# Performance work log

Hardware: AMD Instinct MI355X
Metric: run time of the kernel (lower is better)

The kernel has to match this reference:

```python
import jax, jax.numpy as jnp
import numpy as np

B, S, D, I, C = 4, 512, 512, 1024, 64
BASE_LR = 0.01
EPS = 1e-6


def _rms(x, w):
    return x * jax.lax.rsqrt(jnp.mean(x * x, axis=-1, keepdims=True) + EPS) * w


def _mem_apply(p, x):
    # 2-layer MLP memory: x + RMSNorm(W1 @ silu(W0 @ x))
    h = jax.nn.silu(x @ p["w0"].T)
    y = h @ p["w1"].T
    return x + _rms(y, p["ln"])


def _mem_loss(p, inp, tgt, w):
    # ((target - pred)^2 * theta).mean(-1).sum() over batch; w is scalar theta_t
    pred = _mem_apply(p, inp)
    return jnp.sum(jnp.mean((tgt - pred) ** 2 * w, axis=-1))


def _neural_memory(x, wq, wk, wv, q_norm_w, k_norm_w, alpha_w, alpha_b,
                   theta_w, theta_b, eta_w, eta_b, m_w0, m_w1, m_ln):
    b, s, d = x.shape
    nC = s // C
    params0 = {"w0": m_w0, "w1": m_w1, "ln": m_ln}
    surpr0 = jax.tree_util.tree_map(jnp.zeros_like, params0)
    xs = x.reshape(b, nC, C, d).transpose(1, 0, 2, 3)  # [nC, B, C, D]

    # per-token grads: vmap over sequence dim 1, shared params (in_dims=None)
    grad_fn = jax.vmap(jax.grad(_mem_loss), in_axes=(None, 1, 1, 0))
    idx = jnp.arange(C)

    def step(carry, xc):
        params, surpr = carry
        # adaptive gates: Linear -> sum over batch -> sigmoid (shapes [C])
        al = jax.nn.sigmoid(jnp.sum(xc @ alpha_w.T + alpha_b, axis=0))[:, 0]
        th = jax.nn.sigmoid(jnp.sum(xc @ theta_w.T + theta_b, axis=0))[:, 0] * BASE_LR
        et = jax.nn.sigmoid(jnp.sum(xc @ eta_w.T + eta_b, axis=0))[:, 0]
        k = _rms(jax.nn.silu(xc @ wk.T), k_norm_w)  # [B, C, D]
        v = jax.nn.silu(xc @ wv.T)
        grads = grad_fn(params, k, v, th)  # each leaf [C, *param_shape]
        # eta decay matrix E[m,n] = prod_{i=n+1}^m eta_i for n<=m, else 0
        M0 = jnp.where(idx[:, None] > idx[None, :], et[:, None], 1.0)
        Emat = jnp.where(idx[None, :] <= idx[:, None], jnp.cumprod(M0, axis=0), 0.0)
        c_eta = jnp.cumprod(et)  # prod_{0..m} eta
        beta = 1.0 - al
        bc_last = jnp.cumprod(beta)[-1]
        bt = jnp.cumprod(beta[::-1])[::-1]  # bt[m] = prod_{m..C-1} beta
        w_beta = jnp.concatenate([bt[1:], jnp.ones((1,), et.dtype)])

        def upd(pS, pM, u):
            # S_t = eta_t * S_{t-1} - u_t ; M_t = beta_t * M_{t-1} + S_t (vectorized)
            ex = (slice(None),) + (None,) * pS.ndim
            S_all = c_eta[ex] * pS - jnp.einsum("mn,n...->m...", Emat, u)
            newM = pM * bc_last + jnp.einsum("m,m...->...", w_beta, S_all)
            return newM, S_all[-1]

        res = {n: upd(surpr[n], params[n], grads[n]) for n in params}
        new_params = {n: res[n][0] for n in params}
        new_surpr = {n: res[n][1] for n in params}
        return (new_params, new_surpr), None

    (paramsF, _surprF), _ = jax.lax.scan(step, (params0, surpr0), xs)
    # retrieve from updated memory
    q = _rms(jax.nn.silu(x @ wq.T), q_norm_w)
    return _mem_apply(paramsF, q)


def setup_inputs() -> dict:
    key = jax.random.key(0)
    ks = jax.random.split(key, 12)

    def xavier(k, shape):
        lim = float(np.sqrt(6.0 / (shape[0] + shape[1])))
        return jax.random.uniform(k, shape, jnp.float32, -lim, lim)

    return {
        "x": jax.random.normal(ks[0], (B, S, D), jnp.float32),
        "wq": xavier(ks[1], (D, D)),
        "wk": xavier(ks[2], (D, D)),
        "wv": xavier(ks[3], (D, D)),
        "q_norm_w": jnp.ones((D,), jnp.float32),
        "k_norm_w": jnp.ones((D,), jnp.float32),
        "alpha_w": xavier(ks[4], (1, D)),
        "alpha_b": jnp.zeros((1,), jnp.float32),
        "theta_w": xavier(ks[5], (1, D)),
        "theta_b": jnp.zeros((1,), jnp.float32),
        "eta_w": xavier(ks[6], (1, D)),
        "eta_b": jnp.zeros((1,), jnp.float32),
        "m_w0": xavier(ks[7], (I, D)),
        "m_w1": xavier(ks[8], (D, I)),
        "m_ln": jnp.ones((D,), jnp.float32),
    }


def reference(x, wq, wk, wv, q_norm_w, k_norm_w, alpha_w, alpha_b,
              theta_w, theta_b, eta_w, eta_b, m_w0, m_w1, m_ln):
    return _neural_memory(x, wq, wk, wv, q_norm_w, k_norm_w, alpha_w, alpha_b,
                          theta_w, theta_b, eta_w, eta_b, m_w0, m_w1, m_ln)
```

## Files before the change

kernel.cpp:

```cpp
#include <hip/hip_runtime.h>
#include <math.h>

#define EPS 1e-6f

namespace {

typedef unsigned short u16;
typedef unsigned int u32;
typedef __bf16 bf16x8 __attribute__((ext_vector_type(8)));
typedef float f32x4 __attribute__((ext_vector_type(4)));
typedef u16 u16x8 __attribute__((ext_vector_type(8)));

constexpr int Bb = 4, Ss = 512, Dd = 512, Ii = 1024, Cc = 64;
constexpr int nCk = 8, RowsC = 256, RowsAll = 2048;

__device__ __forceinline__ float sigmoidf_(float x) { return 1.f / (1.f + expf(-x)); }
__device__ __forceinline__ float siluf_(float x)    { return x / (1.f + expf(-x)); }

__device__ __forceinline__ u16 f2bf(float f) {
  u32 u = __float_as_uint(f);
  u32 r = u + 0x7fffu + ((u >> 16) & 1u);
  return (u16)(r >> 16);
}
__device__ __forceinline__ float bf2f(u16 u) {
  return __uint_as_float(((u32)u) << 16);
}

__device__ __forceinline__ void llds16(const u16* g, u16* l) {
  __builtin_amdgcn_global_load_lds((__attribute__((address_space(1))) void*)g,
                                   (__attribute__((address_space(3))) void*)l,
                                   16, 0, 0);
}

__device__ __forceinline__ void drain_barrier() {
  asm volatile("s_waitcnt vmcnt(0)" ::: "memory");
  __builtin_amdgcn_s_barrier();
}

__device__ __forceinline__ float wave_sum(float v) {
  #pragma unroll
  for (int m = 32; m > 0; m >>= 1) v += __shfl_xor(v, m, 64);
  return v;
}

__device__ __forceinline__ float block_reduce_sum(float v, float* red) {
  int tid = threadIdx.x;
  red[tid] = v; __syncthreads();
  for (int s = 128; s > 0; s >>= 1) {
    if (tid < s) red[tid] += red[tid + s];
    __syncthreads();
  }
  float r = red[0]; __syncthreads();
  return r;
}

struct WS {
  float *w0c, *Sw0, *w1c, *Sw1, *lnc, *Sln, *tmpK, *Krows, *Vrows,
        *Ybuf, *gyr, *alv, *thv, *etv, *wBv, *wEv, *scal, *Qb, *Yr;
  u16 *xcb, *wkvqb, *w0b, *w1b, *w1tb, *Kb, *KT, *Hb, *Ht, *dZb,
      *dYb, *dYtW, *dYtE, *dHtW, *dHtE, *Qbb, *Hrb;
};
__host__ __device__ inline WS mkws(char* base) {
  WS s; char* p = base + 256;
#define CF(nm, n) s.nm = (float*)p; p += (size_t)(n) * 4;
#define CU(nm, n) s.nm = (u16*)p;   p += (size_t)(n) * 2;
  CF(w0c, Ii*Dd) CF(Sw0, Ii*Dd) CF(w1c, Dd*Ii) CF(Sw1, Dd*Ii)
  CF(lnc, Dd) CF(Sln, Dd)
  CF(tmpK, (size_t)RowsAll*Dd) CF(Krows, (size_t)RowsAll*Dd) CF(Vrows, (size_t)RowsAll*Dd)
  CF(Ybuf, RowsC*Dd) CF(gyr, RowsC*Dd)
  CF(alv, Ss) CF(thv, Ss) CF(etv, Ss) CF(wBv, nCk*RowsC) CF(wEv, nCk*RowsC) CF(scal, nCk*4)
  CF(Qb, (size_t)RowsAll*Dd) CF(Yr, (size_t)RowsAll*Dd)
  CU(xcb, (size_t)RowsAll*Dd) CU(wkvqb, (size_t)3*Dd*Dd)
  CU(w0b, (size_t)Ii*Dd) CU(w1b, (size_t)2*Dd*Ii) CU(w1tb, (size_t)2*Ii*Dd)
  CU(Kb, (size_t)RowsAll*Dd) CU(KT, (size_t)RowsAll*Dd)
  CU(Hb, RowsC*Ii) CU(Ht, RowsC*Ii) CU(dZb, RowsC*Ii)
  CU(dYb, RowsC*Dd) CU(dYtW, RowsC*Dd) CU(dYtE, RowsC*Dd)
  CU(dHtW, RowsC*Ii) CU(dHtE, RowsC*Ii)
  CU(Qbb, (size_t)RowsAll*Dd) CU(Hrb, (size_t)RowsAll*Ii)
#undef CF
#undef CU
  return s;
}

template<int BK, int NBUF, int EPI>
__device__ void tile64(
    u16* smA, u16* smB,
    const u16* __restrict__ A, const u16* __restrict__ Bt,
    int K, int N, int bm, int bn,
    float* C0, float* C1, float* C2,
    u16* Cb, u16* CbT, u16* CbT2,
    const u16* Zb, const float* wB, const float* wE, int trM)
{
  constexpr int CPR = BK / 8;
  constexpr int NISS = (64 * CPR) / 256;
  constexpr int BUF = 64 * BK;
  const int tid = threadIdx.x;
  const int l = tid & 63, lr = l & 15, lq = l >> 4;
  const int w = tid >> 6, wr = w >> 1, wc = w & 1;

  f32x4 acc[2][2];
  #pragma unroll
  for (int i = 0; i < 2; ++i)
    #pragma unroll
    for (int j = 0; j < 2; ++j) acc[i][j] = f32x4{0.f, 0.f, 0.f, 0.f};

  auto stage = [&](int k0, int buf) {
    u16* dA = smA + buf * BUF;
    u16* dB = smB + buf * BUF;
    #pragma unroll
    for (int i = 0; i < NISS; ++i) {
      int e = i * 256 + tid;
      int r = e / CPR, c = (e & (CPR - 1)) ^ (r & (CPR - 1));
      llds16(A  + (size_t)(bm + r) * K + k0 + c * 8, dA + e * 8);
      llds16(Bt + (size_t)(bn + r) * K + k0 + c * 8, dB + e * 8);
    }
  };

  stage(0, 0);
  drain_barrier();
  const int nt = K / BK;
  int cur = 0;
  for (int t = 0; t < nt; ++t) {
    if (t + 1 < nt) stage((t + 1) * BK, (cur ^ 1) & (NBUF - 1));
    const u16* sA = smA + cur * BUF;
    const u16* sB = smB + cur * BUF;
    #pragma unroll
    for (int kk = 0; kk < BK / 32; ++kk) {
      bf16x8 av[2], bv[2];
      #pragma unroll
      for (int m = 0; m < 2; ++m) {
        int r = wr * 32 + m * 16 + lr;
        int c = (kk * 4 + lq) ^ (r & (CPR - 1));
        av[m] = *reinterpret_cast<const bf16x8*>(&sA[r * BK + c * 8]);
      }
      #pragma unroll
      for (int n = 0; n < 2; ++n) {
        int r = wc * 32 + n * 16 + lr;
        int c = (kk * 4 + lq) ^ (r & (CPR - 1));
        bv[n] = *reinterpret_cast<const bf16x8*>(&sB[r * BK + c * 8]);
      }
      #pragma unroll
      for (int m = 0; m < 2; ++m)
        #pragma unroll
        for (int n = 0; n < 2; ++n)
          acc[m][n] = __builtin_amdgcn_mfma_f32_16x16x32_bf16(av[m], bv[n], acc[m][n], 0, 0, 0);
    }
    drain_barrier();
    cur = (cur ^ 1) & (NBUF - 1);
  }

  #pragma unroll
  for (int m = 0; m < 2; ++m) {
    int gr0 = bm + wr * 32 + m * 16 + lq * 4;
    float wbq[4], weq[4];
    if (EPI == 3) {
      #pragma unroll
      for (int q = 0; q < 4; ++q) { wbq[q] = wB[gr0 + q]; weq[q] = wE[gr0 + q]; }
    }
    #pragma unroll
    for (int n = 0; n < 2; ++n) {
      int gc = bn + wc * 32 + n * 16 + lr;
      ushort4 t1, t2;
      #pragma unroll
      for (int q = 0; q < 4; ++q) {
        float v = acc[m][n][q];
        size_t idx = (size_t)(gr0 + q) * N + gc;
        if (EPI == 0) {
          C0[idx] = v;
        } else if (EPI == 1) {
          size_t rb = (size_t)(gr0 + q) * Dd;
          if (gc < Dd)            C0[rb + gc] = v;
          else if (gc < 2 * Dd)   C1[rb + gc - Dd] = siluf_(v);
          else                    C2[rb + gc - 2 * Dd] = v;
        } else if (EPI == 2) {
          float sg = 1.f / (1.f + expf(-v));
          float h = v * sg;
          float ds = sg * (1.f + v * (1.f - sg));
          Cb[idx] = f2bf(h);
          CbT2[idx] = f2bf(ds);
          ((u16*)&t1)[q] = f2bf(h);
        } else if (EPI == 3) {
          float dh = v * bf2f(Zb[idx]);
          ((u16*)&t1)[q] = f2bf(dh * wbq[q]);
          ((u16*)&t2)[q] = f2bf(dh * weq[q]);
        } else if (EPI == 4) {
          Cb[idx] = f2bf(siluf_(v));
        }
      }
      if (EPI == 2) *reinterpret_cast<ushort4*>(&CbT[(size_t)gc * trM + gr0]) = t1;
      if (EPI == 3) {
        *reinterpret_cast<ushort4*>(&CbT[(size_t)gc * trM + gr0]) = t1;
        *reinterpret_cast<ushort4*>(&CbT2[(size_t)gc * trM + gr0]) = t2;
      }
    }
  }
}

template<int BK, int NBUF, bool TR>
__device__ void gtile64(
    u16* smA, u16* smB, u16* smE,
    const u16* __restrict__ AW, const u16* __restrict__ AE,
    const u16* __restrict__ Bt,
    float* P, float* Sm, u16* Pb, u16* PbT, const float* scal,
    int M, int N, int K, int bm, int bn)
{
  constexpr int CPR = BK / 8;
  constexpr int NISS = (64 * CPR) / 256;
  constexpr int BUF = 64 * BK;
  const int tid = threadIdx.x;
  const int l = tid & 63, lr = l & 15, lq = l >> 4;
  const int w = tid >> 6, wr = w >> 1, wc = w & 1;

  f32x4 aM[2][2], aE[2][2];
  #pragma unroll
  for (int i = 0; i < 2; ++i)
    #pragma unroll
    for (int j = 0; j < 2; ++j) {
      aM[i][j] = f32x4{0.f, 0.f, 0.f, 0.f};
      aE[i][j] = f32x4{0.f, 0.f, 0.f, 0.f};
    }

  auto stage = [&](int k0, int buf) {
    u16* dA = smA + buf * BUF;
    u16* dE = smE + buf * BUF;
    u16* dB = smB + buf * BUF;
    #pragma unroll
    for (int i = 0; i < NISS; ++i) {
      int e = i * 256 + tid;
      int r = e / CPR, c = (e & (CPR - 1)) ^ (r & (CPR - 1));
      llds16(AW + (size_t)(bm + r) * K + k0 + c * 8, dA + e * 8);
      llds16(AE + (size_t)(bm + r) * K + k0 + c * 8, dE + e * 8);
      llds16(Bt + (size_t)(bn + r) * K + k0 + c * 8, dB + e * 8);
    }
  };

  stage(0, 0);
  drain_barrier();
  const int nt = K / BK;
  int cur = 0;
  for (int t = 0; t < nt; ++t) {
    if (t + 1 < nt) stage((t + 1) * BK, (cur ^ 1) & (NBUF - 1));
    const u16* sA = smA + cur * BUF;
    const u16* sE = smE + cur * BUF;
    const u16* sB = smB + cur * BUF;
    #pragma unroll
    for (int kk = 0; kk < BK / 32; ++kk) {
      bf16x8 awv[2], aev[2], bv[2];
      #pragma unroll
      for (int m = 0; m < 2; ++m) {
        int r = wr * 32 + m * 16 + lr;
        int c = (kk * 4 + lq) ^ (r & (CPR - 1));
        awv[m] = *reinterpret_cast<const bf16x8*>(&sA[r * BK + c * 8]);
        aev[m] = *reinterpret_cast<const bf16x8*>(&sE[r * BK + c * 8]);
      }
      #pragma unroll
      for (int n = 0; n < 2; ++n) {
        int r = wc * 32 + n * 16 + lr;
        int c = (kk * 4 + lq) ^ (r & (CPR - 1));
        bv[n] = *reinterpret_cast<const bf16x8*>(&sB[r * BK + c * 8]);
      }
      #pragma unroll
      for (int m = 0; m < 2; ++m)
        #pragma unroll
        for (int n = 0; n < 2; ++n) {
          aM[m][n] = __builtin_amdgcn_mfma_f32_16x16x32_bf16(awv[m], bv[n], aM[m][n], 0, 0, 0);
          aE[m][n] = __builtin_amdgcn_mfma_f32_16x16x32_bf16(aev[m], bv[n], aE[m][n], 0, 0, 0);
        }
    }
    drain_barrier();
    cur = (cur ^ 1) & (NBUF - 1);
  }

  float s0 = scal[0], s1 = scal[1], s2 = scal[2];
  #pragma unroll
  for (int m = 0; m < 2; ++m) {
    int gr0 = bm + wr * 32 + m * 16 + lq * 4;
    #pragma unroll
    for (int n = 0; n < 2; ++n) {
      int gc = bn + wc * 32 + n * 16 + lr;
      ushort4 t1;
      #pragma unroll
      for (int q = 0; q < 4; ++q) {
        size_t idx = (size_t)(gr0 + q) * N + gc;
        float p = P[idx], s = Sm[idx];
        float np = s0 * p + s1 * s - aM[m][n][q];
        float ns = s2 * s - aE[m][n][q];
        P[idx] = np; Sm[idx] = ns;
        Pb[idx] = f2bf(np);
        if (TR) ((u16*)&t1)[q] = f2bf(np);
      }
      if (TR) *reinterpret_cast<ushort4*>(&PbT[(size_t)gc * M + gr0]) = t1;
    }
  }
}


__global__ __launch_bounds__(256) void z0_k(
    const u16* __restrict__ A, const u16* __restrict__ Bt,
    u16* Hb, u16* Ht, u16* dZb)
{
  __shared__ __align__(16) u16 sm[4 * 64 * 128];
  tile64<128, 2, 2>(sm, sm + 2 * 64 * 128, A, Bt, Dd, Ii,
                    blockIdx.y * 64, blockIdx.x * 64,
                    nullptr, nullptr, nullptr, Hb, Ht, dZb,
                    nullptr, nullptr, nullptr, RowsC);
}

__global__ __launch_bounds__(256) void y_k(
    const u16* __restrict__ A, const u16* __restrict__ Bt, float* C0)
{
  __shared__ __align__(16) u16 sm[4 * 64 * 128];
  tile64<128, 2, 0>(sm, sm + 2 * 64 * 128, A, Bt, Ii, Dd,
                    blockIdx.y * 64, blockIdx.x * 64,
                    C0, nullptr, nullptr, nullptr, nullptr, nullptr,
                    nullptr, nullptr, nullptr, 0);
}

__global__ __launch_bounds__(256) void s4_k(
    const u16* __restrict__ dYb, const u16* __restrict__ w1t_cur,
    const u16* __restrict__ dZb, u16* dHtW, u16* dHtE,
    const float* __restrict__ gyr, float* lnc, float* Sln,
    const u16* __restrict__ dYtW, const u16* __restrict__ dYtE,
    const u16* __restrict__ Ht,
    float* w1c, float* Sw1, u16* w1b_new, u16* w1t_new,
    const float* wB, const float* wE, const float* scal)
{
  __shared__ __align__(16) u16 sm[6 * 64 * 128];
  int j = blockIdx.x;
  if (j < 64) {
    int tm = j & 3, tn = j >> 2;
    tile64<128, 2, 3>(sm, sm + 2 * 64 * 128, dYb, w1t_cur, Dd, Ii,
                      tm * 64, tn * 64,
                      nullptr, nullptr, nullptr, nullptr, dHtW, dHtE,
                      dZb, wB, wE, RowsC);
  } else if (j < 66) {
    int d = (j - 64) * 256 + threadIdx.x;
    float sm2 = 0.f, se2 = 0.f;
    for (int r = 0; r < RowsC; ++r) {
      float vv = gyr[(size_t)r * Dd + d];
      sm2 += wB[r] * vv; se2 += wE[r] * vv;
    }
    float pp = lnc[d], sn = Sln[d];
    lnc[d] = scal[0] * pp + scal[1] * sn - sm2;
    Sln[d] = scal[2] * sn - se2;
  } else {
    int q = j - 66;
    gtile64<128, 2, true>(sm, sm + 2 * 64 * 128, sm + 4 * 64 * 128,
                          dYtW, dYtE, Ht, w1c, Sw1, w1b_new, w1t_new,
                          scal, Dd, Ii, RowsC, (q >> 4) * 64, (q & 15) * 64);
  }
}

__global__ __launch_bounds__(256) void g2b_k(
    const u16* __restrict__ dHtW, const u16* __restrict__ dHtE,
    const u16* __restrict__ KTc,
    float* w0c, float* Sw0, u16* w0b, const float* scal)
{
  __shared__ __align__(16) u16 sm[6 * 64 * 128];
  int j = blockIdx.x;
  gtile64<128, 2, false>(sm, sm + 2 * 64 * 128, sm + 4 * 64 * 128,
                         dHtW, dHtE, KTc, w0c, Sw0, w0b, nullptr,
                         scal, Ii, Dd, RowsC, (j >> 3) * 64, (j & 7) * 64);
}

__global__ __launch_bounds__(256) void kvq_k(
    const u16* __restrict__ xcb, const u16* __restrict__ wkvqb,
    float* tmpK, float* Vrows, float* Yq, char* ws)
{
  __shared__ __align__(16) u16 sm[4 * 64 * 128];
  int j = blockIdx.x;
  if (j < 768) {
    int tn = j % 24, tm = j / 24;
    tile64<128, 2, 1>(sm, sm + 2 * 64 * 128, xcb, wkvqb, Dd, 3 * Dd,
                      tm * 64, tn * 64,
                      tmpK, Vrows, Yq, nullptr, nullptr, nullptr,
                      nullptr, nullptr, nullptr, 0);
    return;
  }
  if (threadIdx.x != 0) return;
  WS S = mkws(ws);
  int ci = j - 768;
  const float* alc = S.alv + ci * Cc;
  const float* etc_ = S.etv + ci * Cc;
  float beta[Cc], wb[Cc], ce[Cc], E[Cc], T[Cc];
  for (int i = 0; i < Cc; ++i) beta[i] = 1.f - alc[i];
  wb[Cc - 1] = 1.f;
  for (int m = Cc - 2; m >= 0; --m) wb[m] = wb[m + 1] * beta[m + 1];
  float bc_last = wb[0] * beta[0];
  float p = 1.f, A = 0.f;
  for (int m = 0; m < Cc; ++m) { p *= etc_[m]; ce[m] = p; A += wb[m] * ce[m]; }
  E[Cc - 1] = 1.f; T[Cc - 1] = 1.f;
  for (int n = Cc - 2; n >= 0; --n) {
    E[n] = E[n + 1] * etc_[n + 1];
    T[n] = wb[n] + etc_[n + 1] * T[n + 1];
  }
  for (int b = 0; b < Bb; ++b)
    for (int t = 0; t < Cc; ++t) {
      S.wBv[ci * RowsC + b * Cc + t] = T[t];
      S.wEv[ci * RowsC + b * Cc + t] = E[t];
    }
  S.scal[ci * 4 + 0] = bc_last; S.scal[ci * 4 + 1] = A; S.scal[ci * 4 + 2] = ce[Cc - 1];
}

template<int EPI>
__global__ __launch_bounds__(256) void mgemm128_k(
    const u16* __restrict__ A, const u16* __restrict__ Bt,
    float* C0, u16* Cb, int M, int N, int K)
{
  constexpr int TS = 128, BK = 64;
  constexpr int BUF = TS * BK;
  __shared__ __align__(16) u16 As[2 * BUF];
  __shared__ __align__(16) u16 Bs[2 * BUF];
  const int tid = threadIdx.x;
  const int l = tid & 63, lr = l & 15, lq = l >> 4;
  const int w = tid >> 6, wr = w >> 1, wc = w & 1;
  const int bm = blockIdx.y * TS, bn = blockIdx.x * TS;

  f32x4 acc[4][4];
  #pragma unroll
  for (int i = 0; i < 4; ++i)
    #pragma unroll
    for (int j = 0; j < 4; ++j) acc[i][j] = f32x4{0.f, 0.f, 0.f, 0.f};

  auto stage = [&](int k0, int buf) {
    u16* dA = As + buf * BUF;
    u16* dB = Bs + buf * BUF;
    #pragma unroll
    for (int i = 0; i < 4; ++i) {
      int e = i * 256 + tid;
      int r = e >> 3, c = (e & 7) ^ (r & 7);
      llds16(A  + (size_t)(bm + r) * K + k0 + c * 8, dA + e * 8);
      llds16(Bt + (size_t)(bn + r) * K + k0 + c * 8, dB + e * 8);
    }
  };

  stage(0, 0);
  drain_barrier();
  const int nt = K / BK;
  int cur = 0;
  for (int t = 0; t < nt; ++t) {
    if (t + 1 < nt) stage((t + 1) * BK, cur ^ 1);
    const u16* sA = As + cur * BUF;
    const u16* sB = Bs + cur * BUF;
    #pragma unroll
    for (int kk = 0; kk < 2; ++kk) {
      bf16x8 av[4], bv[4];
      #pragma unroll
      for (int m = 0; m < 4; ++m) {
        int r = wr * 64 + m * 16 + lr;
        int c = (kk * 4 + lq) ^ (r & 7);
        av[m] = *reinterpret_cast<const bf16x8*>(&sA[r * BK + c * 8]);
      }
      #pragma unroll
      for (int n = 0; n < 4; ++n) {
        int r = wc * 64 + n * 16 + lr;
        int c = (kk * 4 + lq) ^ (r & 7);
        bv[n] = *reinterpret_cast<const bf16x8*>(&sB[r * BK + c * 8]);
      }
      #pragma unroll
      for (int m = 0; m < 4; ++m)
        #pragma unroll
        for (int n = 0; n < 4; ++n)
          acc[m][n] = __builtin_amdgcn_mfma_f32_16x16x32_bf16(av[m], bv[n], acc[m][n], 0, 0, 0);
    }
    drain_barrier();
    cur ^= 1;
  }

  #pragma unroll
  for (int m = 0; m < 4; ++m) {
    int gr0 = bm + wr * 64 + m * 16 + lq * 4;
    #pragma unroll
    for (int n = 0; n < 4; ++n) {
      int gc = bn + wc * 64 + n * 16 + lr;
      #pragma unroll
      for (int q = 0; q < 4; ++q) {
        size_t idx = (size_t)(gr0 + q) * N + gc;
        float v = acc[m][n][q];
        if (EPI == 0) C0[idx] = v;
        else          Cb[idx] = f2bf(siluf_(v));
      }
    }
  }
}

__global__ __launch_bounds__(256) void init_k(
    const float* __restrict__ x,
    const float* __restrict__ aw, const float* __restrict__ ab,
    const float* __restrict__ tw, const float* __restrict__ tb,
    const float* __restrict__ ew, const float* __restrict__ eb,
    const float* __restrict__ wq, const float* __restrict__ wkw,
    const float* __restrict__ wvw, const float* __restrict__ mw0,
    const float* __restrict__ mw1, const float* __restrict__ mln,
    char* ws)
{
  WS S = mkws(ws);
  const int tid = threadIdx.x;
  if (blockIdx.x < 512) {
    __shared__ float red[256];
    int s = blockIdx.x;
    int ci = s >> 6, t = s & 63;
    float sa = 0.f, st = 0.f, se = 0.f;
    for (int b = 0; b < Bb; ++b) {
      const float* xr = x + ((size_t)b * Ss + s) * Dd;
      u16* dst = S.xcb + ((size_t)(ci * RowsC + b * Cc + t)) * Dd;
      for (int d = tid; d < Dd; d += 256) {
        float v = xr[d];
        dst[d] = f2bf(v);
        sa += v * aw[d]; st += v * tw[d]; se += v * ew[d];
      }
    }
    sa = block_reduce_sum(sa, red);
    st = block_reduce_sum(st, red);
    se = block_reduce_sum(se, red);
    if (tid == 0) {
      S.alv[s] = sigmoidf_(sa + Bb * ab[0]);
      S.thv[s] = sigmoidf_(st + Bb * tb[0]) * 0.01f;
      S.etv[s] = sigmoidf_(se + Bb * eb[0]);
    }
    return;
  }
  if (blockIdx.x < 640) {
    __shared__ float t[64][65];
    int tt = blockIdx.x - 512;
    int br = (tt & 7) * 64, bc = (tt >> 3) * 64;
    #pragma unroll
    for (int i = 0; i < 16; ++i) {
      int e = tid + i * 256;
      int r = e >> 6, c = e & 63;
      t[r][c] = mw1[(size_t)(br + r) * Ii + bc + c];
    }
    __syncthreads();
    #pragma unroll
    for (int i = 0; i < 16; ++i) {
      int e = tid + i * 256;
      int rr = e >> 6, cc = e & 63;
      S.w1tb[(size_t)(bc + rr) * Dd + br + cc] = f2bf(t[cc][rr]);
    }
    return;
  }
  const int i0 = (blockIdx.x - 640) * 256 + tid;
  const int stride = 512 * 256;
  for (int i = i0; i < (Dd * Dd) / 4; i += stride) {
    float4 v = ((const float4*)wkw)[i];
    ushort4 o; o.x = f2bf(v.x); o.y = f2bf(v.y); o.z = f2bf(v.z); o.w = f2bf(v.w);
    ((ushort4*)S.wkvqb)[i] = o;
    v = ((const float4*)wvw)[i];
    o.x = f2bf(v.x); o.y = f2bf(v.y); o.z = f2bf(v.z); o.w = f2bf(v.w);
    ((ushort4*)S.wkvqb)[i + (Dd * Dd) / 4] = o;
    v = ((const float4*)wq)[i];
    o.x = f2bf(v.x); o.y = f2bf(v.y); o.z = f2bf(v.z); o.w = f2bf(v.w);
    ((ushort4*)S.wkvqb)[i + (Dd * Dd) / 2] = o;
  }
  for (int i = i0; i < (Ii * Dd) / 4; i += stride) {
    float4 z4; z4.x = z4.y = z4.z = z4.w = 0.f;
    float4 v = ((const float4*)mw0)[i];
    ((float4*)S.w0c)[i] = v; ((float4*)S.Sw0)[i] = z4;
    ushort4 o; o.x = f2bf(v.x); o.y = f2bf(v.y); o.z = f2bf(v.z); o.w = f2bf(v.w);
    ((ushort4*)S.w0b)[i] = o;
    v = ((const float4*)mw1)[i];
    ((float4*)S.w1c)[i] = v; ((float4*)S.Sw1)[i] = z4;
    o.x = f2bf(v.x); o.y = f2bf(v.y); o.z = f2bf(v.z); o.w = f2bf(v.w);
    ((ushort4*)S.w1b)[i] = o;
  }
  for (int i = i0; i < Dd; i += stride) { S.lnc[i] = mln[i]; S.Sln[i] = 0.f; }
}

__global__ __launch_bounds__(256) void norm2_k(
    const float* __restrict__ tmpK, const float* __restrict__ Yq,
    float* Krows, u16* Kb, u16* KT,
    float* Qb, u16* Qbb,
    const float* __restrict__ kn, const float* __restrict__ qn)
{
  __shared__ u16 lt[4][Dd];
  const int tid = threadIdx.x, w = tid >> 6, l = tid & 63;
  const bool isQ = blockIdx.x >= 512;
  const int r0 = (isQ ? (int)blockIdx.x - 512 : (int)blockIdx.x) * 4;
  const int row = r0 + w, d0 = l * 8;
  const float* in = (isQ ? Yq : tmpK) + (size_t)row * Dd + d0;
  const float* nw = (isQ ? qn : kn) + d0;
  float v[8];
  *(float4*)&v[0] = *(const float4*)in;
  *(float4*)&v[4] = *(const float4*)(in + 4);
  float ss = 0.f;
  #pragma unroll
  for (int j = 0; j < 8; ++j) { v[j] = siluf_(v[j]); ss += v[j] * v[j]; }
  ss = wave_sum(ss);
  float rr = rsqrtf(ss / (float)Dd + EPS);
  float nv[8];
  *(float4*)&nv[0] = *(const float4*)nw;
  *(float4*)&nv[4] = *(const float4*)(nw + 4);
  float y[8]; u16x8 pb;
  #pragma unroll
  for (int j = 0; j < 8; ++j) { y[j] = v[j] * rr * nv[j]; pb[j] = f2bf(y[j]); }
  float* outf = (isQ ? Qb : Krows) + (size_t)row * Dd + d0;
  u16* outb = (isQ ? Qbb : Kb) + (size_t)row * Dd + d0;
  *(float4*)outf       = *(float4*)&y[0];
  *(float4*)(outf + 4) = *(float4*)&y[4];
  *(u16x8*)outb = pb;
  if (!isQ) {
    int ci = r0 >> 8, rloc = r0 & 255;
    u16* KTc = KT + (size_t)ci * Dd * RowsC;
    #pragma unroll
    for (int j = 0; j < 8; ++j) lt[w][d0 + j] = pb[j];
    __syncthreads();
    for (int d = tid; d < Dd; d += 256) {
      ushort4 pk;
      pk.x = lt[0][d]; pk.y = lt[1][d]; pk.z = lt[2][d]; pk.w = lt[3][d];
      *reinterpret_cast<ushort4*>(&KTc[(size_t)d * RowsC + rloc]) = pk;
    }
  }
}

__global__ __launch_bounds__(256) void loss_back4_k(
    const float* __restrict__ Kr, const float* __restrict__ Vr,
    const float* __restrict__ Y, const float* __restrict__ lnc,
    const float* __restrict__ th, const float* __restrict__ wB,
    const float* __restrict__ wE,
    u16* __restrict__ dYb, u16* __restrict__ dYtW, u16* __restrict__ dYtE,
    float* __restrict__ gyr)
{
  __shared__ u16 lw[4][Dd];
  __shared__ u16 le[4][Dd];
  const int tid = threadIdx.x, w = tid >> 6, l = tid & 63;
  const int row = blockIdx.x * 4 + w, t = row & 63, d0 = l * 8;
  size_t base = (size_t)row * Dd + d0;

  float y[8], kk[8], vv[8], lv[8];
  *(float4*)&y[0]  = *(const float4*)(Y + base);
  *(float4*)&y[4]  = *(const float4*)(Y + base + 4);
  *(float4*)&kk[0] = *(const float4*)(Kr + base);
  *(float4*)&kk[4] = *(const float4*)(Kr + base + 4);
  *(float4*)&vv[0] = *(const float4*)(Vr + base);
  *(float4*)&vv[4] = *(const float4*)(Vr + base + 4);
  *(float4*)&lv[0] = *(const float4*)(lnc + d0);
  *(float4*)&lv[4] = *(const float4*)(lnc + d0 + 4);

  float ss = 0.f;
  #pragma unroll
  for (int q = 0; q < 8; ++q) ss += y[q] * y[q];
  ss = wave_sum(ss);
  float rr = rsqrtf(ss / (float)Dd + EPS);
  float c = 2.f * th[t] / (float)Dd;

  float g[8], s2 = 0.f;
  #pragma unroll
  for (int q = 0; q < 8; ++q) {
    g[q] = c * ((kk[q] + y[q] * rr * lv[q]) - vv[q]);
    s2 += g[q] * lv[q] * y[q];
  }
  s2 = wave_sum(s2);
  float coef = rr * rr * rr * s2 / (float)Dd;

  float wb = wB[row], we = wE[row];
  u16x8 pb; float gy[8];
  #pragma unroll
  for (int q = 0; q < 8; ++q) {
    float dv = rr * g[q] * lv[q] - coef * y[q];
    pb[q] = f2bf(dv);
    lw[w][d0 + q] = f2bf(dv * wb);
    le[w][d0 + q] = f2bf(dv * we);
    gy[q] = g[q] * y[q] * rr;
  }
  *(u16x8*)(dYb + base) = pb;
  *(float4*)(gyr + base)     = *(float4*)&gy[0];
  *(float4*)(gyr + base + 4) = *(float4*)&gy[4];

  __syncthreads();
  int r0 = blockIdx.x * 4;
  for (int d = tid; d < Dd; d += 256) {
    ushort4 pw, pe;
    pw.x = lw[0][d]; pw.y = lw[1][d]; pw.z = lw[2][d]; pw.w = lw[3][d];
    pe.x = le[0][d]; pe.y = le[1][d]; pe.z = le[2][d]; pe.w = le[3][d];
    *reinterpret_cast<ushort4*>(&dYtW[(size_t)d * RowsC + r0]) = pw;
    *reinterpret_cast<ushort4*>(&dYtE[(size_t)d * RowsC + r0]) = pe;
  }
}

__global__ __launch_bounds__(256) void final4_k(
    const float* __restrict__ Q, const float* __restrict__ Y,
    const float* __restrict__ lnc, float* __restrict__ out)
{
  const int tid = threadIdx.x, w = tid >> 6, l = tid & 63;
  const int row = blockIdx.x * 4 + w;
  const int ci = row >> 8, wi = row & 255, b = wi >> 6, t = wi & 63;
  const int d0 = l * 8;
  const float* yr = Y + (size_t)row * Dd + d0;
  float y[8];
  *(float4*)&y[0] = *(const float4*)yr;
  *(float4*)&y[4] = *(const float4*)(yr + 4);
  float ss = 0.f;
  #pragma unroll
  for (int q = 0; q < 8; ++q) ss += y[q] * y[q];
  ss = wave_sum(ss);
  float rr = rsqrtf(ss / (float)Dd + EPS);
  const float* qb = Q + (size_t)row * Dd + d0;
  const float* lf = lnc + d0;
  float o[8];
  #pragma unroll
  for (int q = 0; q < 8; ++q) o[q] = qb[q] + y[q] * rr * lf[q];
  float* ob = out + ((size_t)b * Ss + ci * Cc + t) * Dd + d0;
  *(float4*)ob       = *(float4*)&o[0];
  *(float4*)(ob + 4) = *(float4*)&o[4];
}

}

extern "C" void kernel_launch(void* const* d_in, const int* in_sizes, int n_in,
                              void* d_out, int out_size, void* d_ws, size_t ws_size,
                              hipStream_t stream)
{
  const float* x   = (const float*)d_in[0];
  const float* wq  = (const float*)d_in[1];
  const float* wkw = (const float*)d_in[2];
  const float* wvw = (const float*)d_in[3];
  const float* qn  = (const float*)d_in[4];
  const float* kn  = (const float*)d_in[5];
  const float* aw  = (const float*)d_in[6];
  const float* ab  = (const float*)d_in[7];
  const float* tw  = (const float*)d_in[8];
  const float* tb  = (const float*)d_in[9];
  const float* ew  = (const float*)d_in[10];
  const float* eb  = (const float*)d_in[11];
  const float* mw0 = (const float*)d_in[12];
  const float* mw1 = (const float*)d_in[13];
  const float* mln = (const float*)d_in[14];
  float* out = (float*)d_out;
  char* ws = (char*)d_ws;
  WS S = mkws(ws);

  init_k<<<1152, 256, 0, stream>>>(x, aw, ab, tw, tb, ew, eb,
                                   wq, wkw, wvw, mw0, mw1, mln, ws);
  kvq_k<<<776, 256, 0, stream>>>(S.xcb, S.wkvqb, S.tmpK, S.Vrows, S.Yr, ws);
  norm2_k<<<1024, 256, 0, stream>>>(S.tmpK, S.Yr, S.Krows, S.Kb, S.KT,
                                    S.Qb, S.Qbb, kn, qn);

  for (int ci = 0; ci < nCk; ++ci) {
    const int p = ci & 1;
    const u16* Kbc = S.Kb + (size_t)ci * RowsC * Dd;
    const u16* KTc = S.KT + (size_t)ci * Dd * RowsC;
    const float* Krc = S.Krows + (size_t)ci * RowsC * Dd;
    const float* Vrc = S.Vrows + (size_t)ci * RowsC * Dd;
    const float* scc = S.scal + ci * 4;
    const float* wBc = S.wBv + ci * RowsC;
    const float* wEc = S.wEv + ci * RowsC;
    const float* thc = S.thv + ci * Cc;
    u16* w1b_cur = S.w1b + (size_t)p * Dd * Ii;
    u16* w1b_new = S.w1b + (size_t)(p ^ 1) * Dd * Ii;
    u16* w1t_cur = S.w1tb + (size_t)p * Ii * Dd;
    u16* w1t_new = S.w1tb + (size_t)(p ^ 1) * Ii * Dd;

    z0_k<<<dim3(Ii / 64, RowsC / 64), 256, 0, stream>>>(
        Kbc, S.w0b, S.Hb, S.Ht, S.dZb);
    y_k<<<dim3(Dd / 64, RowsC / 64), 256, 0, stream>>>(
        S.Hb, w1b_cur, S.Ybuf);
    loss_back4_k<<<RowsC / 4, 256, 0, stream>>>(
        Krc, Vrc, S.Ybuf, S.lnc, thc, wBc, wEc, S.dYb, S.dYtW, S.dYtE, S.gyr);
    s4_k<<<194, 256, 0, stream>>>(
        S.dYb, w1t_cur, S.dZb, S.dHtW, S.dHtE, S.gyr, S.lnc, S.Sln,
        S.dYtW, S.dYtE, S.Ht, S.w1c, S.Sw1, w1b_new, w1t_new,
        wBc, wEc, scc);
    g2b_k<<<128, 256, 0, stream>>>(
        S.dHtW, S.dHtE, KTc, S.w0c, S.Sw0, S.w0b, scc);
  }

  mgemm128_k<4><<<dim3(Ii / 128, RowsAll / 128), 256, 0, stream>>>(
      S.Qbb, S.w0b, nullptr, S.Hrb, RowsAll, Ii, Dd);
  mgemm128_k<0><<<dim3(Dd / 128, RowsAll / 128), 256, 0, stream>>>(
      S.Hrb, S.w1b, S.Yr, nullptr, RowsAll, Dd, Ii);
  final4_k<<<RowsAll / 4, 256, 0, stream>>>(S.Qb, S.Yr, S.lnc, out);
}
```

Baseline: 394.9 us.

## Fuse hidden-layer GEMM and output GEMM per chunk with split-K partial sums

Merges the z0 (K·W0ᵀ with SiLU epilogue) and y (H·W1ᵀ) kernels into one kernel. Each block computes a 64x64 H tile, keeps it in shared memory, and multiplies it by the matching 64-column slice of W1 to produce a full-width partial Y. Sixteen partials are written to a scratch buffer and summed in loss_back4_k. This removes one launch and the H round trip through global memory. In exchange it writes and reads 16x more fp32 Y partial data, and the second GEMM runs on only 64 blocks with large register accumulators.

```diff
diff --git a/kernel.cpp b/kernel.cpp
--- a/kernel.cpp
+++ b/kernel.cpp
@@ -56,8 +56,8 @@
 
 struct WS {
   float *w0c, *Sw0, *w1c, *Sw1, *lnc, *Sln, *tmpK, *Krows, *Vrows,
-        *Ybuf, *gyr, *alv, *thv, *etv, *wBv, *wEv, *scal, *Qb, *Yr;
-  u16 *xcb, *wkvqb, *w0b, *w1b, *w1tb, *Kb, *KT, *Hb, *Ht, *dZb,
+        *Yp, *gyr, *alv, *thv, *etv, *wBv, *wEv, *scal, *Qb, *Yr;
+  u16 *xcb, *wkvqb, *w0b, *w1b, *w1tb, *Kb, *KT, *Ht, *dZb,
       *dYb, *dYtW, *dYtE, *dHtW, *dHtE, *Qbb, *Hrb;
 };
 __host__ __device__ inline WS mkws(char* base) {
@@ -67,13 +67,13 @@
   CF(w0c, Ii*Dd) CF(Sw0, Ii*Dd) CF(w1c, Dd*Ii) CF(Sw1, Dd*Ii)
   CF(lnc, Dd) CF(Sln, Dd)
   CF(tmpK, (size_t)RowsAll*Dd) CF(Krows, (size_t)RowsAll*Dd) CF(Vrows, (size_t)RowsAll*Dd)
-  CF(Ybuf, RowsC*Dd) CF(gyr, RowsC*Dd)
+  CF(Yp, (size_t)16*RowsC*Dd) CF(gyr, RowsC*Dd)
   CF(alv, Ss) CF(thv, Ss) CF(etv, Ss) CF(wBv, nCk*RowsC) CF(wEv, nCk*RowsC) CF(scal, nCk*4)
   CF(Qb, (size_t)RowsAll*Dd) CF(Yr, (size_t)RowsAll*Dd)
   CU(xcb, (size_t)RowsAll*Dd) CU(wkvqb, (size_t)3*Dd*Dd)
   CU(w0b, (size_t)Ii*Dd) CU(w1b, (size_t)2*Dd*Ii) CU(w1tb, (size_t)2*Ii*Dd)
   CU(Kb, (size_t)RowsAll*Dd) CU(KT, (size_t)RowsAll*Dd)
-  CU(Hb, RowsC*Ii) CU(Ht, RowsC*Ii) CU(dZb, RowsC*Ii)
+  CU(Ht, RowsC*Ii) CU(dZb, RowsC*Ii)
   CU(dYb, RowsC*Dd) CU(dYtW, RowsC*Dd) CU(dYtE, RowsC*Dd)
   CU(dHtW, RowsC*Ii) CU(dHtE, RowsC*Ii)
   CU(Qbb, (size_t)RowsAll*Dd) CU(Hrb, (size_t)RowsAll*Ii)
@@ -88,7 +88,7 @@
     const u16* __restrict__ A, const u16* __restrict__ Bt,
     int K, int N, int bm, int bn,
     float* C0, float* C1, float* C2,
-    u16* Cb, u16* CbT, u16* CbT2,
+    u16* CbT, u16* CbT2,
     const u16* Zb, const float* wB, const float* wE, int trM)
 {
   constexpr int CPR = BK / 8;
@@ -172,22 +172,12 @@
           if (gc < Dd)            C0[rb + gc] = v;
           else if (gc < 2 * Dd)   C1[rb + gc - Dd] = siluf_(v);
           else                    C2[rb + gc - 2 * Dd] = v;
-        } else if (EPI == 2) {
-          float sg = 1.f / (1.f + expf(-v));
-          float h = v * sg;
-          float ds = sg * (1.f + v * (1.f - sg));
-          Cb[idx] = f2bf(h);
-          CbT2[idx] = f2bf(ds);
-          ((u16*)&t1)[q] = f2bf(h);
         } else if (EPI == 3) {
           float dh = v * bf2f(Zb[idx]);
           ((u16*)&t1)[q] = f2bf(dh * wbq[q]);
           ((u16*)&t2)[q] = f2bf(dh * weq[q]);
-        } else if (EPI == 4) {
-          Cb[idx] = f2bf(siluf_(v));
         }
       }
-      if (EPI == 2) *reinterpret_cast<ushort4*>(&CbT[(size_t)gc * trM + gr0]) = t1;
       if (EPI == 3) {
         *reinterpret_cast<ushort4*>(&CbT[(size_t)gc * trM + gr0]) = t1;
         *reinterpret_cast<ushort4*>(&CbT2[(size_t)gc * trM + gr0]) = t2;
@@ -295,25 +285,147 @@
 }
 
 
-__global__ __launch_bounds__(256) void z0_k(
-    const u16* __restrict__ A, const u16* __restrict__ Bt,
-    u16* Hb, u16* Ht, u16* dZb)
-{
-  __shared__ __align__(16) u16 sm[4 * 64 * 128];
-  tile64<128, 2, 2>(sm, sm + 2 * 64 * 128, A, Bt, Dd, Ii,
-                    blockIdx.y * 64, blockIdx.x * 64,
-                    nullptr, nullptr, nullptr, Hb, Ht, dZb,
-                    nullptr, nullptr, nullptr, RowsC);
-}
-
-__global__ __launch_bounds__(256) void y_k(
-    const u16* __restrict__ A, const u16* __restrict__ Bt, float* C0)
-{
-  __shared__ __align__(16) u16 sm[4 * 64 * 128];
-  tile64<128, 2, 0>(sm, sm + 2 * 64 * 128, A, Bt, Ii, Dd,
-                    blockIdx.y * 64, blockIdx.x * 64,
-                    C0, nullptr, nullptr, nullptr, nullptr, nullptr,
-                    nullptr, nullptr, nullptr, 0);
+__global__ __launch_bounds__(256) void z0y_k(
+    const u16* __restrict__ Kbc, const u16* __restrict__ w0b,
+    const u16* __restrict__ w1b,
+    u16* __restrict__ Ht, u16* __restrict__ dZb, float* __restrict__ Yp)
+{
+  __shared__ __align__(16) u16 sm[4 * 64 * 128 + 64 * 64];
+  u16* Hs = sm + 4 * 64 * 128;
+  const int tid = threadIdx.x;
+  const int l = tid & 63, lr = l & 15, lq = l >> 4;
+  const int w = tid >> 6, wr = w >> 1, wc = w & 1;
+  const int tj = blockIdx.x, tr = blockIdx.y;
+  const int bm = tr * 64, bn = tj * 64;
+
+  {
+    constexpr int BK = 128, CPR = 16, NISS = 4, BUF = 64 * BK;
+    u16* smA = sm; u16* smB = sm + 2 * BUF;
+    f32x4 acc[2][2];
+    #pragma unroll
+    for (int i = 0; i < 2; ++i)
+      #pragma unroll
+      for (int j = 0; j < 2; ++j) acc[i][j] = f32x4{0.f, 0.f, 0.f, 0.f};
+
+    auto stage = [&](int k0, int buf) {
+      u16* dA = smA + buf * BUF;
+      u16* dB = smB + buf * BUF;
+      #pragma unroll
+      for (int i = 0; i < NISS; ++i) {
+        int e = i * 256 + tid;
+        int r = e / CPR, c = (e & (CPR - 1)) ^ (r & (CPR - 1));
+        llds16(Kbc + (size_t)(bm + r) * Dd + k0 + c * 8, dA + e * 8);
+        llds16(w0b + (size_t)(bn + r) * Dd + k0 + c * 8, dB + e * 8);
+      }
+    };
+    stage(0, 0);
+    drain_barrier();
+    int cur = 0;
+    for (int t = 0; t < 4; ++t) {
+      if (t + 1 < 4) stage((t + 1) * BK, cur ^ 1);
+      const u16* sA = smA + cur * BUF;
+      const u16* sB = smB + cur * BUF;
+      #pragma unroll
+      for (int kk = 0; kk < 4; ++kk) {
+        bf16x8 av[2], bv[2];
+        #pragma unroll
+        for (int m = 0; m < 2; ++m) {
+          int r = wr * 32 + m * 16 + lr;
+          int c = (kk * 4 + lq) ^ (r & (CPR - 1));
+          av[m] = *reinterpret_cast<const bf16x8*>(&sA[r * BK + c * 8]);
+        }
+        #pragma unroll
+        for (int n = 0; n < 2; ++n) {
+          int r = wc * 32 + n * 16 + lr;
+          int c = (kk * 4 + lq) ^ (r & (CPR - 1));
+          bv[n] = *reinterpret_cast<const bf16x8*>(&sB[r * BK + c * 8]);
+        }
+        #pragma unroll
+        for (int m = 0; m < 2; ++m)
+          #pragma unroll
+          for (int n = 0; n < 2; ++n)
+            acc[m][n] = __builtin_amdgcn_mfma_f32_16x16x32_bf16(av[m], bv[n], acc[m][n], 0, 0, 0);
+      }
+      drain_barrier();
+      cur ^= 1;
+    }
+
+    #pragma unroll
+    for (int i = 0; i < 16; ++i) {
+      int e = i * 256 + tid;
+      int r = e >> 3, c = (e & 7) ^ (r & 7);
+      llds16(w1b + (size_t)r * Ii + bn + c * 8, sm + e * 8);
+    }
+
+    #pragma unroll
+    for (int m = 0; m < 2; ++m) {
+      int gr0 = bm + wr * 32 + m * 16 + lq * 4;
+      int rl0 = wr * 32 + m * 16 + lq * 4;
+      #pragma unroll
+      for (int n = 0; n < 2; ++n) {
+        int gc = bn + wc * 32 + n * 16 + lr;
+        int cl = wc * 32 + n * 16 + lr;
+        ushort4 t1;
+        #pragma unroll
+        for (int q = 0; q < 4; ++q) {
+          float v = acc[m][n][q];
+          float sg = 1.f / (1.f + expf(-v));
+          float h = v * sg;
+          float ds = sg * (1.f + v * (1.f - sg));
+          u16 hb = f2bf(h);
+          ((u16*)&t1)[q] = hb;
+          dZb[(size_t)(gr0 + q) * Ii + gc] = f2bf(ds);
+          int rl = rl0 + q;
+          Hs[rl * 64 + ((((cl >> 3) ^ (rl & 7)) << 3) | (cl & 7))] = hb;
+        }
+        *reinterpret_cast<ushort4*>(&Ht[(size_t)gc * RowsC + gr0]) = t1;
+      }
+    }
+  }
+
+  asm volatile("s_waitcnt vmcnt(0)" ::: "memory");
+  __syncthreads();
+
+  {
+    f32x4 yacc[2][16];
+    #pragma unroll
+    for (int m = 0; m < 2; ++m)
+      #pragma unroll
+      for (int n = 0; n < 16; ++n) yacc[m][n] = f32x4{0.f, 0.f, 0.f, 0.f};
+
+    #pragma unroll
+    for (int kk = 0; kk < 2; ++kk) {
+      bf16x8 av[2];
+      #pragma unroll
+      for (int m = 0; m < 2; ++m) {
+        int r = wr * 32 + m * 16 + lr;
+        int c = (kk * 4 + lq) ^ (r & 7);
+        av[m] = *reinterpret_cast<const bf16x8*>(&Hs[r * 64 + c * 8]);
+      }
+      #pragma unroll
+      for (int n = 0; n < 16; ++n) {
+        int r = wc * 256 + n * 16 + lr;
+        int c = (kk * 4 + lq) ^ (r & 7);
+        bf16x8 bv = *reinterpret_cast<const bf16x8*>(&sm[r * 64 + c * 8]);
+        #pragma unroll
+        for (int m = 0; m < 2; ++m)
+          yacc[m][n] = __builtin_amdgcn_mfma_f32_16x16x32_bf16(av[m], bv, yacc[m][n], 0, 0, 0);
+      }
+    }
+
+    float* Yo = Yp + (size_t)tj * RowsC * Dd;
+    #pragma unroll
+    for (int m = 0; m < 2; ++m) {
+      int gr0 = bm + wr * 32 + m * 16 + lq * 4;
+      #pragma unroll
+      for (int n = 0; n < 16; ++n) {
+        int gc = wc * 256 + n * 16 + lr;
+        #pragma unroll
+        for (int q = 0; q < 4; ++q)
+          Yo[(size_t)(gr0 + q) * Dd + gc] = yacc[m][n][q];
+      }
+    }
+  }
 }
 
 __global__ __launch_bounds__(256) void s4_k(
@@ -331,7 +443,7 @@
     int tm = j & 3, tn = j >> 2;
     tile64<128, 2, 3>(sm, sm + 2 * 64 * 128, dYb, w1t_cur, Dd, Ii,
                       tm * 64, tn * 64,
-                      nullptr, nullptr, nullptr, nullptr, dHtW, dHtE,
+                      nullptr, nullptr, nullptr, dHtW, dHtE,
                       dZb, wB, wE, RowsC);
   } else if (j < 66) {
     int d = (j - 64) * 256 + threadIdx.x;
@@ -373,7 +485,7 @@
     int tn = j % 24, tm = j / 24;
     tile64<128, 2, 1>(sm, sm + 2 * 64 * 128, xcb, wkvqb, Dd, 3 * Dd,
                       tm * 64, tn * 64,
-                      tmpK, Vrows, Yq, nullptr, nullptr, nullptr,
+                      tmpK, Vrows, Yq, nullptr, nullptr,
                       nullptr, nullptr, nullptr, 0);
     return;
   }
@@ -614,7 +726,7 @@
 
 __global__ __launch_bounds__(256) void loss_back4_k(
     const float* __restrict__ Kr, const float* __restrict__ Vr,
-    const float* __restrict__ Y, const float* __restrict__ lnc,
+    const float* __restrict__ Yp, const float* __restrict__ lnc,
     const float* __restrict__ th, const float* __restrict__ wB,
     const float* __restrict__ wE,
     u16* __restrict__ dYb, u16* __restrict__ dYtW, u16* __restrict__ dYtE,
@@ -626,9 +738,17 @@
   const int row = blockIdx.x * 4 + w, t = row & 63, d0 = l * 8;
   size_t base = (size_t)row * Dd + d0;
 
-  float y[8], kk[8], vv[8], lv[8];
-  *(float4*)&y[0]  = *(const float4*)(Y + base);
-  *(float4*)&y[4]  = *(const float4*)(Y + base + 4);
+  float y[8] = {0.f, 0.f, 0.f, 0.f, 0.f, 0.f, 0.f, 0.f};
+  #pragma unroll
+  for (int p2 = 0; p2 < 16; ++p2) {
+    const float* yp = Yp + (size_t)p2 * (RowsC * Dd) + base;
+    float4 u0 = *(const float4*)yp;
+    float4 u1 = *(const float4*)(yp + 4);
+    y[0] += u0.x; y[1] += u0.y; y[2] += u0.z; y[3] += u0.w;
+    y[4] += u1.x; y[5] += u1.y; y[6] += u1.z; y[7] += u1.w;
+  }
+
+  float kk[8], vv[8], lv[8];
   *(float4*)&kk[0] = *(const float4*)(Kr + base);
   *(float4*)&kk[4] = *(const float4*)(Kr + base + 4);
   *(float4*)&vv[0] = *(const float4*)(Vr + base);
@@ -750,12 +870,10 @@
     u16* w1t_cur = S.w1tb + (size_t)p * Ii * Dd;
     u16* w1t_new = S.w1tb + (size_t)(p ^ 1) * Ii * Dd;
 
-    z0_k<<<dim3(Ii / 64, RowsC / 64), 256, 0, stream>>>(
-        Kbc, S.w0b, S.Hb, S.Ht, S.dZb);
-    y_k<<<dim3(Dd / 64, RowsC / 64), 256, 0, stream>>>(
-        S.Hb, w1b_cur, S.Ybuf);
+    z0y_k<<<dim3(16, 4), 256, 0, stream>>>(
+        Kbc, S.w0b, w1b_cur, S.Ht, S.dZb, S.Yp);
     loss_back4_k<<<RowsC / 4, 256, 0, stream>>>(
-        Krc, Vrc, S.Ybuf, S.lnc, thc, wBc, wEc, S.dYb, S.dYtW, S.dYtE, S.gyr);
+        Krc, Vrc, S.Yp, S.lnc, thc, wBc, wEc, S.dYb, S.dYtW, S.dYtE, S.gyr);
     s4_k<<<194, 256, 0, stream>>>(
         S.dYb, w1t_cur, S.dZb, S.dHtW, S.dHtE, S.gyr, S.lnc, S.Sln,
         S.dYtW, S.dYtE, S.Ht, S.w1c, S.Sw1, w1b_new, w1t_new,
```

After: 385.6 us, median of 2. 2.4% less time.
